# Optimization experiments

Measured on AMD Instinct MI355X. Metric: run time of the kernel, lower is better.

## Reference

```python
import jax, jax.numpy as jnp
import numpy as np

RADIUS = 0.2
NSAMPLE = 32


def ball_query(new_xyz, xyz, radius, nsample):
    # new_xyz: (B, M, 3), xyz: (B, N, 3) -> idx: (B, M, nsample) int32
    B, M, _ = new_xyz.shape
    N = xyz.shape[1]
    # pairwise squared distances (B, M, N)
    diff = new_xyz[:, :, None, :] - xyz[:, None, :, :]
    dist2 = jnp.sum(diff * diff, axis=-1)
    mask = dist2 < (radius * radius)
    ar = jnp.arange(N, dtype=jnp.int32)
    masked = jnp.where(mask, ar[None, None, :], jnp.int32(N + 1))  # (B,M,N)
    sorted_idx = jnp.sort(masked, axis=2)[:, :, :nsample]          # (B,M,nsample)
    invalid = sorted_idx >= N
    first = sorted_idx[:, :, 0:1]
    idx = jnp.where(invalid, jnp.broadcast_to(first, sorted_idx.shape), sorted_idx)
    return idx


def group_points(points, idx):
    # points: (B, C, N), idx: (B, M, nsample) -> (B, C, M, nsample)
    B, C, N = points.shape
    M, ns = idx.shape[1], idx.shape[2]
    flat = jnp.broadcast_to(idx.reshape(B, 1, M * ns), (B, C, M * ns))
    return jnp.take_along_axis(points, flat, axis=2).reshape(B, C, M, ns)


def setup_inputs() -> dict:
    key = jax.random.key(0)
    k1, k2, k3 = jax.random.split(key, 3)
    xyz = jax.random.uniform(k1, (8, 16384, 3), dtype=jnp.float32)
    new_xyz = jax.random.uniform(k2, (8, 1024, 3), dtype=jnp.float32)
    features = jax.random.normal(k3, (8, 64, 16384), dtype=jnp.float32)
    return {"xyz": xyz, "new_xyz": new_xyz, "features": features}


def reference(xyz, new_xyz, features):
    idx = ball_query(new_xyz, xyz, RADIUS, NSAMPLE)          # (B,M,ns)
    xyz_t = jnp.transpose(xyz, (0, 2, 1))                    # (B,3,N)
    grouped_xyz = group_points(xyz_t, idx)                   # (B,3,M,ns)
    grouped_xyz = grouped_xyz - jnp.transpose(new_xyz, (0, 2, 1))[:, :, :, None]
    grouped_features = group_points(features, idx)           # (B,C,M,ns)
    new_features = jnp.concatenate([grouped_xyz, grouped_features], axis=1)
    return new_features                                      # (B, 3+C, M, ns)
```

## Files before the change

### kernel.cpp

```cpp
#include <hip/hip_runtime.h>


#define N_PTS   16384
#define M_Q     1024
#define B_SZ    8
#define NSAMP   32
#define NCH     64
#define R2      0.04f
#define OUT_CH  (3 + NCH)

typedef float f4 __attribute__((ext_vector_type(4)));

#define GLDS4(gp, lp)                                                        \
    __builtin_amdgcn_global_load_lds(                                        \
        (const __attribute__((address_space(1))) unsigned int*)(gp),         \
        (__attribute__((address_space(3))) unsigned int*)(lp), 4, 0, 0)

__global__ __launch_bounds__(256, 8) void transpose_kernel(
    const float* __restrict__ feat, const float* __restrict__ xyz,
    float* __restrict__ ft,
    float* __restrict__ xs, float* __restrict__ ys, float* __restrict__ zs)
{
    __shared__ float tile[64][65];
    const int b   = blockIdx.x & 7;
    const int n0  = (blockIdx.x >> 3) << 6;
    const int tid = threadIdx.x;
    const float* __restrict__ fb = feat + (size_t)b * NCH * N_PTS;
    float* __restrict__ tb       = ft   + ((size_t)b * N_PTS + n0) * NCH;

    if (xs && tid < 64) {
        const int p = n0 + tid;
        const float* src = xyz + ((size_t)b * N_PTS + p) * 3;
        xs[(size_t)b * N_PTS + p] = src[0];
        ys[(size_t)b * N_PTS + p] = src[1];
        zs[(size_t)b * N_PTS + p] = src[2];
    }

#pragma unroll
    for (int j = 0; j < 4; ++j) {
        const int fidx = j * 256 + tid;
        const int c = fidx >> 4;
        const int q = fidx & 15;
        const f4 v = __builtin_nontemporal_load(
            (const f4*)&fb[(size_t)c * N_PTS + n0 + q * 4]);
        tile[c][q * 4 + 0] = v.x;
        tile[c][q * 4 + 1] = v.y;
        tile[c][q * 4 + 2] = v.z;
        tile[c][q * 4 + 3] = v.w;
    }
    __syncthreads();
    const int c4 = tid & 15;
    const int r  = tid >> 4;
#pragma unroll
    for (int j = 0; j < 4; ++j) {
        const int nn = j * 16 + r;
        f4 o;
        o.x = tile[c4 * 4 + 0][nn];
        o.y = tile[c4 * 4 + 1][nn];
        o.z = tile[c4 * 4 + 2][nn];
        o.w = tile[c4 * 4 + 3][nn];
        *(f4*)(&tb[(size_t)nn * NCH + c4 * 4]) = o;
    }
}

template <bool SOA>
__global__ __launch_bounds__(256, 8) void qg_main(
    const float* __restrict__ xyz,
    const float* __restrict__ new_xyz,
    const float* __restrict__ ft,
    const float* __restrict__ xs, const float* __restrict__ ys,
    const float* __restrict__ zs,
    float* __restrict__ out)
{
    const int tid  = threadIdx.x;
    const int w    = tid >> 6;
    const int lane = tid & 63;
    const int b    = blockIdx.x & 7;
    const int m    = ((blockIdx.x >> 3) << 2) + w;
    const int q    = (b << 10) + m;

    __shared__ float pxyz[4][NSAMP][4];
    __shared__ float tile[4][32][32];

    const float cx = new_xyz[q * 3 + 0];
    const float cy = new_xyz[q * 3 + 1];
    const float cz = new_xyz[q * 3 + 2];
    const float* __restrict__ xb = xyz + (size_t)b * N_PTS * 3;
    const unsigned long long lmask = (1ull << lane) - 1ull;
    int cnt = 0;

    if constexpr (SOA) {
        const f4* __restrict__ xs4 = (const f4*)(xs + (size_t)b * N_PTS);
        const f4* __restrict__ ys4 = (const f4*)(ys + (size_t)b * N_PTS);
        const f4* __restrict__ zs4 = (const f4*)(zs + (size_t)b * N_PTS);

        f4 X = xs4[lane], Y = ys4[lane], Z = zs4[lane];

        for (int base = 0; ; base += 256) {
            const int  nbase = base + 256;
            const bool more  = nbase < N_PTS;
            const int  pidx  = more ? (nbase >> 2) + lane : lane;
            const f4 NX = xs4[pidx], NY = ys4[pidx], NZ = zs4[pidx];

            float d2k[4];
#pragma unroll
            for (int k = 0; k < 4; ++k) {
                const float dx = __fsub_rn(cx, X[k]);
                const float dy = __fsub_rn(cy, Y[k]);
                const float dz = __fsub_rn(cz, Z[k]);
                d2k[k] = __fadd_rn(__fadd_rn(__fmul_rn(dx, dx), __fmul_rn(dy, dy)),
                                   __fmul_rn(dz, dz));
            }
            const bool h0 = d2k[0] < R2, h1 = d2k[1] < R2;
            const bool h2 = d2k[2] < R2, h3 = d2k[3] < R2;
            const unsigned long long m0 = __ballot(h0);
            const unsigned long long m1 = __ballot(h1);
            const unsigned long long m2 = __ballot(h2);
            const unsigned long long m3 = __ballot(h3);

            const int P = (int)(__popcll(m0 & lmask) + __popcll(m1 & lmask) +
                                __popcll(m2 & lmask) + __popcll(m3 & lmask));
            int own = 0;
            const bool hk[4] = {h0, h1, h2, h3};
#pragma unroll
            for (int k = 0; k < 4; ++k) {
                if (hk[k]) {
                    const int slot = cnt + P + own;
                    if (slot < NSAMP) {
                        pxyz[w][slot][0] = X[k];
                        pxyz[w][slot][1] = Y[k];
                        pxyz[w][slot][2] = Z[k];
                        pxyz[w][slot][3] = __int_as_float(base + lane * 4 + k);
                    }
                }
                own += hk[k] ? 1 : 0;
            }
            cnt += (int)(__popcll(m0) + __popcll(m1) + __popcll(m2) + __popcll(m3));

            if (cnt >= NSAMP || !more) break;
            X = NX; Y = NY; Z = NZ;
        }
    } else {
        float Ax = xb[lane * 3 + 0], Ay = xb[lane * 3 + 1], Az = xb[lane * 3 + 2];
        float Bx = xb[(64 + lane) * 3 + 0], By = xb[(64 + lane) * 3 + 1],
              Bz = xb[(64 + lane) * 3 + 2];

        for (int base = 0; ; base += 128) {
            const int  nbase = base + 128;
            const bool more  = nbase < N_PTS;
            const int  pA = more ? nbase + lane : lane;
            const int  pB = pA + 64;
            const float nAx = xb[pA * 3 + 0], nAy = xb[pA * 3 + 1], nAz = xb[pA * 3 + 2];
            const float nBx = xb[pB * 3 + 0], nBy = xb[pB * 3 + 1], nBz = xb[pB * 3 + 2];

            {
                const float dx = __fsub_rn(cx, Ax), dy = __fsub_rn(cy, Ay), dz = __fsub_rn(cz, Az);
                const float d2 = __fadd_rn(__fadd_rn(__fmul_rn(dx, dx), __fmul_rn(dy, dy)),
                                           __fmul_rn(dz, dz));
                const bool hit = d2 < R2;
                const unsigned long long mk = __ballot(hit);
                if (hit) {
                    const int slot = cnt + __popcll(mk & lmask);
                    if (slot < NSAMP) {
                        pxyz[w][slot][0] = Ax; pxyz[w][slot][1] = Ay;
                        pxyz[w][slot][2] = Az; pxyz[w][slot][3] = __int_as_float(base + lane);
                    }
                }
                cnt += (int)__popcll(mk);
            }
            {
                const float dx = __fsub_rn(cx, Bx), dy = __fsub_rn(cy, By), dz = __fsub_rn(cz, Bz);
                const float d2 = __fadd_rn(__fadd_rn(__fmul_rn(dx, dx), __fmul_rn(dy, dy)),
                                           __fmul_rn(dz, dz));
                const bool hit = d2 < R2;
                const unsigned long long mk = __ballot(hit);
                if (hit) {
                    const int slot = cnt + __popcll(mk & lmask);
                    if (slot < NSAMP) {
                        pxyz[w][slot][0] = Bx; pxyz[w][slot][1] = By;
                        pxyz[w][slot][2] = Bz; pxyz[w][slot][3] = __int_as_float(base + 64 + lane);
                    }
                }
                cnt += (int)__popcll(mk);
            }
            if (cnt >= NSAMP || !more) break;
            Ax = nAx; Ay = nAy; Az = nAz;
            Bx = nBx; By = nBy; Bz = nBz;
        }
    }

    if (lane < NSAMP && cnt < NSAMP) {
        float v0x, v0y, v0z, v0w;
        if (cnt > 0) {
            v0x = pxyz[w][0][0]; v0y = pxyz[w][0][1];
            v0z = pxyz[w][0][2]; v0w = pxyz[w][0][3];
        } else {
            v0x = xb[0]; v0y = xb[1]; v0z = xb[2]; v0w = __int_as_float(0);
        }
        if (lane >= cnt) {
            pxyz[w][lane][0] = v0x; pxyz[w][lane][1] = v0y;
            pxyz[w][lane][2] = v0z; pxyz[w][lane][3] = v0w;
        }
    }

    float* __restrict__ ob = out + ((size_t)b * OUT_CH * M_Q + (size_t)m) * NSAMP;
    const float* __restrict__ ftb = ft + (size_t)b * N_PTS * NCH;

    const int half = lane >> 5;
    const int c5   = lane & 31;

#pragma unroll
    for (int t = 0; t < 16; ++t) {
        const int s   = 2 * t + half;
        const int ns  = __float_as_int(pxyz[w][s][3]);
        const int col = c5 ^ ((2 * t) & 28);
        GLDS4(ftb + (size_t)ns * NCH + col, &tile[w][2 * t][0]);
    }

    if (lane < 24) {
        const int c  = lane >> 3;
        const int s4 = lane & 7;
        const float ctr = (c == 0) ? cx : ((c == 1) ? cy : cz);
        f4 o;
        o.x = __fsub_rn(pxyz[w][s4 * 4 + 0][c], ctr);
        o.y = __fsub_rn(pxyz[w][s4 * 4 + 1][c], ctr);
        o.z = __fsub_rn(pxyz[w][s4 * 4 + 2][c], ctr);
        o.w = __fsub_rn(pxyz[w][s4 * 4 + 3][c], ctr);
        __builtin_nontemporal_store(o, (f4*)&ob[(size_t)c * (M_Q * NSAMP) + s4 * 4]);
    }

    const int cl = (lane >> 3);
    const int s4 = lane & 7;
    const int xr = s4 * 4;

    asm volatile("s_waitcnt vmcnt(0)" ::: "memory");
    __builtin_amdgcn_sched_barrier(0);
#pragma unroll
    for (int j = 0; j < 4; ++j) {
        const int c_loc = j * 8 + cl;
        f4 o;
        o.x = tile[w][xr + 0][c_loc ^ xr];
        o.y = tile[w][xr + 1][c_loc ^ xr];
        o.z = tile[w][xr + 2][c_loc ^ xr];
        o.w = tile[w][xr + 3][c_loc ^ xr];
        __builtin_nontemporal_store(
            o, (f4*)&ob[(size_t)(3 + c_loc) * (M_Q * NSAMP) + s4 * 4]);
    }

    asm volatile("s_waitcnt lgkmcnt(0)" ::: "memory");
    __builtin_amdgcn_sched_barrier(0);
#pragma unroll
    for (int t = 0; t < 16; ++t) {
        const int s   = 2 * t + half;
        const int ns  = __float_as_int(pxyz[w][s][3]);
        const int col = c5 ^ ((2 * t) & 28);
        GLDS4(ftb + (size_t)ns * NCH + 32 + col, &tile[w][2 * t][0]);
    }
    asm volatile("s_waitcnt vmcnt(0)" ::: "memory");
    __builtin_amdgcn_sched_barrier(0);
#pragma unroll
    for (int j = 0; j < 4; ++j) {
        const int c_loc = j * 8 + cl;
        f4 o;
        o.x = tile[w][xr + 0][c_loc ^ xr];
        o.y = tile[w][xr + 1][c_loc ^ xr];
        o.z = tile[w][xr + 2][c_loc ^ xr];
        o.w = tile[w][xr + 3][c_loc ^ xr];
        __builtin_nontemporal_store(
            o, (f4*)&ob[(size_t)(3 + 32 + c_loc) * (M_Q * NSAMP) + s4 * 4]);
    }
}

__global__ __launch_bounds__(256) void qg_fallback(
    const float* __restrict__ xyz, const float* __restrict__ new_xyz,
    const float* __restrict__ feat, float* __restrict__ out)
{
    const int tid  = threadIdx.x;
    const int w    = tid >> 6;
    const int lane = tid & 63;
    const int q    = blockIdx.x * 4 + w;
    const int b    = q >> 10;
    const int m    = q & (M_Q - 1);

    __shared__ int idx_sh[4][NSAMP];

    const float cx = new_xyz[q * 3 + 0];
    const float cy = new_xyz[q * 3 + 1];
    const float cz = new_xyz[q * 3 + 2];
    const float* __restrict__ xb = xyz + (size_t)b * N_PTS * 3;

    int cnt = 0;
    for (int base = 0; base < N_PTS && cnt < NSAMP; base += 64) {
        const int n = base + lane;
        const float dx = __fsub_rn(cx, xb[n * 3 + 0]);
        const float dy = __fsub_rn(cy, xb[n * 3 + 1]);
        const float dz = __fsub_rn(cz, xb[n * 3 + 2]);
        const float d2 = __fadd_rn(__fadd_rn(__fmul_rn(dx, dx), __fmul_rn(dy, dy)),
                                   __fmul_rn(dz, dz));
        const bool hit = d2 < R2;
        const unsigned long long mk = __ballot(hit);
        if (hit) {
            const int slot = cnt + __popcll(mk & ((1ull << lane) - 1ull));
            if (slot < NSAMP) idx_sh[w][slot] = n;
        }
        cnt += (int)__popcll(mk);
    }
    __syncthreads();
    if (lane < NSAMP) {
        const int v0 = (cnt > 0) ? idx_sh[w][0] : 0;
        if (lane >= cnt) idx_sh[w][lane] = v0;
    }
    __syncthreads();

    const float* __restrict__ fb = feat + (size_t)b * NCH * N_PTS;
    float* __restrict__ ob = out + ((size_t)b * OUT_CH * M_Q + (size_t)m) * NSAMP;
    for (int e = lane; e < OUT_CH * NSAMP; e += 64) {
        const int c = e >> 5, s = e & 31;
        const int n = idx_sh[w][s];
        float v;
        if (c < 3) {
            const float ctr = (c == 0) ? cx : ((c == 1) ? cy : cz);
            v = __fsub_rn(xb[n * 3 + c], ctr);
        } else {
            v = fb[(size_t)(c - 3) * N_PTS + n];
        }
        ob[(size_t)c * (M_Q * NSAMP) + s] = v;
    }
}

extern "C" void kernel_launch(void* const* d_in, const int* in_sizes, int n_in,
                              void* d_out, int out_size, void* d_ws, size_t ws_size,
                              hipStream_t stream) {
    const float* xyz     = (const float*)d_in[0];
    const float* new_xyz = (const float*)d_in[1];
    const float* feat    = (const float*)d_in[2];
    float* out           = (float*)d_out;

    const size_t ft_elems  = (size_t)B_SZ * N_PTS * NCH;
    const size_t soa_elems = (size_t)B_SZ * N_PTS;
    const size_t need_soa  = (ft_elems + 3 * soa_elems) * sizeof(float);
    const size_t need_ft   = ft_elems * sizeof(float);

    float* ft = (float*)d_ws;
    float* xs = ft + ft_elems;
    float* ys = xs + soa_elems;
    float* zs = ys + soa_elems;

    if (ws_size >= need_soa) {
        transpose_kernel<<<B_SZ * (N_PTS / 64), 256, 0, stream>>>(feat, xyz, ft, xs, ys, zs);
        qg_main<true><<<(B_SZ * M_Q) / 4, 256, 0, stream>>>(
            xyz, new_xyz, ft, xs, ys, zs, out);
    } else if (ws_size >= need_ft) {
        transpose_kernel<<<B_SZ * (N_PTS / 64), 256, 0, stream>>>(
            feat, xyz, ft, nullptr, nullptr, nullptr);
        qg_main<false><<<(B_SZ * M_Q) / 4, 256, 0, stream>>>(
            xyz, new_xyz, ft, nullptr, nullptr, nullptr, out);
    } else {
        qg_fallback<<<(B_SZ * M_Q) / 4, 256, 0, stream>>>(xyz, new_xyz, feat, out);
    }
}
```

Measured before the change: 121.9 us.

## Stage SoA point chunks in double-buffered LDS shared across waves in ball query

The ball-query scan no longer has each wave load its own xs/ys/zs vectors from global memory. The block now cooperatively streams 256-point chunks into a double-buffered LDS area (aliased onto the existing tile buffer) using global_load_lds. All four waves, whose queries share the same batch, read from that one copy. This cuts redundant global and cache traffic, but adds a block-wide barrier per chunk. Waves now advance in lockstep, so a block keeps scanning until its slowest query has found enough neighbours.

```diff
diff --git a/kernel.cpp b/kernel.cpp
--- a/kernel.cpp
+++ b/kernel.cpp
@@ -8,6 +8,7 @@
 #define NCH     64
 #define R2      0.04f
 #define OUT_CH  (3 + NCH)
+#define NCHUNK  (N_PTS / 256)
 
 typedef float f4 __attribute__((ext_vector_type(4)));
 
@@ -81,6 +82,7 @@
 
     __shared__ float pxyz[4][NSAMP][4];
     __shared__ float tile[4][32][32];
+    float (*scan)[3][256] = reinterpret_cast<float(*)[3][256]>(&tile[0][0][0]);
 
     const float cx = new_xyz[q * 3 + 0];
     const float cy = new_xyz[q * 3 + 1];
@@ -90,17 +92,32 @@
     int cnt = 0;
 
     if constexpr (SOA) {
-        const f4* __restrict__ xs4 = (const f4*)(xs + (size_t)b * N_PTS);
-        const f4* __restrict__ ys4 = (const f4*)(ys + (size_t)b * N_PTS);
-        const f4* __restrict__ zs4 = (const f4*)(zs + (size_t)b * N_PTS);
-
-        f4 X = xs4[lane], Y = ys4[lane], Z = zs4[lane];
-
-        for (int base = 0; ; base += 256) {
-            const int  nbase = base + 256;
-            const bool more  = nbase < N_PTS;
-            const int  pidx  = more ? (nbase >> 2) + lane : lane;
-            const f4 NX = xs4[pidx], NY = ys4[pidx], NZ = zs4[pidx];
+        const float* __restrict__ xsb = xs + (size_t)b * N_PTS;
+        const float* __restrict__ ysb = ys + (size_t)b * N_PTS;
+        const float* __restrict__ zsb = zs + (size_t)b * N_PTS;
+
+        {
+            const int off = w * 64 + lane;
+            GLDS4(xsb + off, &scan[0][0][w * 64]);
+            GLDS4(ysb + off, &scan[0][1][w * 64]);
+            GLDS4(zsb + off, &scan[0][2][w * 64]);
+        }
+        asm volatile("s_waitcnt vmcnt(0)" ::: "memory");
+        __syncthreads();
+
+        int cur = 0;
+        for (int t = 0; ; ++t) {
+            const bool more = (t + 1) < NCHUNK;
+            if (more) {
+                const int off = (t + 1) * 256 + w * 64 + lane;
+                GLDS4(xsb + off, &scan[cur ^ 1][0][w * 64]);
+                GLDS4(ysb + off, &scan[cur ^ 1][1][w * 64]);
+                GLDS4(zsb + off, &scan[cur ^ 1][2][w * 64]);
+            }
+
+            const f4 X = *(const f4*)&scan[cur][0][lane * 4];
+            const f4 Y = *(const f4*)&scan[cur][1][lane * 4];
+            const f4 Z = *(const f4*)&scan[cur][2][lane * 4];
 
             float d2k[4];
 #pragma unroll
@@ -130,15 +147,17 @@
                         pxyz[w][slot][0] = X[k];
                         pxyz[w][slot][1] = Y[k];
                         pxyz[w][slot][2] = Z[k];
-                        pxyz[w][slot][3] = __int_as_float(base + lane * 4 + k);
+                        pxyz[w][slot][3] = __int_as_float(t * 256 + lane * 4 + k);
                     }
                 }
                 own += hk[k] ? 1 : 0;
             }
             cnt += (int)(__popcll(m0) + __popcll(m1) + __popcll(m2) + __popcll(m3));
 
-            if (cnt >= NSAMP || !more) break;
-            X = NX; Y = NY; Z = NZ;
+            const bool mydone = (cnt >= NSAMP) || !more;
+            asm volatile("s_waitcnt vmcnt(0)" ::: "memory");
+            if (__syncthreads_and((int)mydone)) break;
+            cur ^= 1;
         }
     } else {
         float Ax = xb[lane * 3 + 0], Ay = xb[lane * 3 + 1], Az = xb[lane * 3 + 2];
```

New measurement: 134.5 us. 1.1x slower.
